# Performance work log

Measured on AMD Instinct MI355X. Metric: run time of the kernel, lower is better.

## Reference

```python
import jax, jax.numpy as jnp
import numpy as np


def setup_inputs() -> dict:
    key = jax.random.key(0)
    k1, k2, k3, k4 = jax.random.split(key, 4)
    N, E, F_IN, H, C = 100000, 1600000, 128, 64, 64
    x = jax.random.normal(k1, (N, F_IN), dtype=jnp.float32)
    edge_index = jax.random.randint(k2, (2, E), 0, N, dtype=jnp.int64)
    W1 = jax.random.normal(k3, (F_IN, H), dtype=jnp.float32) / np.sqrt(F_IN)
    b1 = jnp.zeros((H,), dtype=jnp.float32)
    W2 = jax.random.normal(k4, (H, C), dtype=jnp.float32) / np.sqrt(H)
    b2 = jnp.zeros((C,), dtype=jnp.float32)
    return {"x": x, "edge_index": edge_index, "W1": W1, "b1": b1, "W2": W2, "b2": b2}


def reference(x, edge_index, W1, b1, W2, b2):
    N = x.shape[0]
    # add self-loops (PyG GCNConv default)
    loop = jnp.arange(N, dtype=edge_index.dtype)
    src = jnp.concatenate([edge_index[0], loop])
    dst = jnp.concatenate([edge_index[1], loop])
    # symmetric normalization: deg^{-1/2}[src] * deg^{-1/2}[dst], deg over dst
    deg = jax.ops.segment_sum(jnp.ones_like(dst, dtype=x.dtype), dst, num_segments=N)
    dis = jnp.where(deg > 0, jax.lax.rsqrt(deg), 0.0)
    norm = dis[src] * dis[dst]  # [E+N]

    def gcn_conv(h, W, b):
        h = h @ W                                   # [N, out]
        msg = h[src] * norm[:, None]                # [E+N, out] gather
        agg = jax.ops.segment_sum(msg, dst, num_segments=N)  # scatter-add
        return agg + b

    h = jax.nn.relu(gcn_conv(x, W1, b1))
    # dropout inactive in eval mode
    out = gcn_conv(h, W2, b2)
    return jax.nn.log_softmax(out, axis=1)
```

## Files before the change

kernel.cpp:

```cpp
#include <hip/hip_runtime.h>
#include <cstdint>
#include <cstddef>

#define PASSA_EDGES 8192
#define PASSB_CAP   12288

typedef __attribute__((ext_vector_type(8))) short bf16x8;
typedef __attribute__((ext_vector_type(4))) float f32x4;


__device__ __forceinline__ unsigned short f2bf(float f) {
    unsigned int u = __float_as_uint(f);
    u += 0x7FFFu + ((u >> 16) & 1u);
    return (unsigned short)(u >> 16);
}
__device__ __forceinline__ float bf2f(unsigned short h) {
    return __uint_as_float((unsigned int)h << 16);
}

__device__ __forceinline__ void bf8_fma(uint4 u, float w, float* acc) {
    acc[0] += __uint_as_float(u.x << 16) * w;
    acc[1] += __uint_as_float(u.x & 0xFFFF0000u) * w;
    acc[2] += __uint_as_float(u.y << 16) * w;
    acc[3] += __uint_as_float(u.y & 0xFFFF0000u) * w;
    acc[4] += __uint_as_float(u.z << 16) * w;
    acc[5] += __uint_as_float(u.z & 0xFFFF0000u) * w;
    acc[6] += __uint_as_float(u.w << 16) * w;
    acc[7] += __uint_as_float(u.w & 0xFFFF0000u) * w;
}
__device__ __forceinline__ void bf8_unpack(uint4 u, float* v) {
    v[0] = __uint_as_float(u.x << 16);
    v[1] = __uint_as_float(u.x & 0xFFFF0000u);
    v[2] = __uint_as_float(u.y << 16);
    v[3] = __uint_as_float(u.y & 0xFFFF0000u);
    v[4] = __uint_as_float(u.z << 16);
    v[5] = __uint_as_float(u.z & 0xFFFF0000u);
    v[6] = __uint_as_float(u.w << 16);
    v[7] = __uint_as_float(u.w & 0xFFFF0000u);
}


__global__ void bcur_init(int* __restrict__ bcur, int NBUCK, int CAP) {
    int b = threadIdx.x;
    if (b < NBUCK) bcur[b] = b * CAP;
}


__global__ __launch_bounds__(256) void passA(const int* __restrict__ src,
                                             const int* __restrict__ dst,
                                             int* __restrict__ bcur,
                                             int2* __restrict__ bbuf, int E,
                                             int CAP, int shift) {
    __shared__ int2 bins[PASSA_EDGES];
    __shared__ int  cnt[256], off[256], cur[256], gbase[256];
    const int t  = threadIdx.x;
    const int e0 = blockIdx.x * PASSA_EDGES;
    const int n  = min(PASSA_EDGES, E - e0);

    cnt[t] = 0;
    __syncthreads();
    for (int i = t; i < n; i += 256) atomicAdd(&cnt[dst[e0 + i] >> shift], 1);
    __syncthreads();

    int v = cnt[t];
    off[t] = v;
    __syncthreads();
    for (int o = 1; o < 256; o <<= 1) {
        int u = (t >= o) ? off[t - o] : 0;
        __syncthreads();
        off[t] += u;
        __syncthreads();
    }
    int excl = off[t] - v;
    off[t]   = excl;
    cur[t]   = excl;
    __syncthreads();

    for (int i = t; i < n; i += 256) {
        int d = dst[e0 + i];
        int s = src[e0 + i];
        int p = atomicAdd(&cur[d >> shift], 1);
        bins[p] = make_int2(s, d);
    }
    if (cnt[t] > 0) gbase[t] = atomicAdd(&bcur[t], cnt[t]);
    __syncthreads();

    const int w = t >> 6, lane = t & 63;
    for (int b = w; b < 256; b += 4) {
        int c = cnt[b];
        if (c == 0) continue;
        int lo  = off[b], go = gbase[b];
        int lim = (b + 1) * CAP;
        if (go + c > lim) c = max(0, lim - go);
        for (int i = lane; i < c; i += 64) bbuf[go + i] = bins[lo + i];
    }
}


__global__ __launch_bounds__(256) void hist_dis(const int2* __restrict__ bbuf,
                                                const int* __restrict__ bcur,
                                                int* __restrict__ hist,
                                                float* __restrict__ dis,
                                                int N, int CAP, int shift) {
    __shared__ int cnt[1024];
    const int b     = blockIdx.x;
    const int node0 = b << shift;
    const int nn    = min(1 << shift, N - node0);
    for (int j = threadIdx.x; j < nn; j += 256) cnt[j] = 0;
    __syncthreads();
    const int start = b * CAP, end = bcur[b];
    for (int e = start + threadIdx.x; e < end; e += 256)
        atomicAdd(&cnt[bbuf[e].y - node0], 1);
    __syncthreads();
    for (int j = threadIdx.x; j < nn; j += 256) {
        int c = cnt[j];
        hist[node0 + j] = (c + 7) & ~7;
        dis[node0 + j]  = rsqrtf((float)(c + 1));
    }
}


__global__ __launch_bounds__(256) void scan_partial(const int* __restrict__ hist,
                                                    int* __restrict__ partials, int N) {
    __shared__ int red[256];
    const int t    = threadIdx.x;
    const int base = blockIdx.x * 1024 + t * 4;
    int s = 0;
    if (base + 3 < N) {
        int4 v = *(const int4*)&hist[base];
        s = v.x + v.y + v.z + v.w;
    } else {
        for (int i = 0; i < 4; i++)
            if (base + i < N) s += hist[base + i];
    }
    red[t] = s;
    __syncthreads();
    for (int off = 128; off; off >>= 1) {
        if (t < off) red[t] += red[t + off];
        __syncthreads();
    }
    if (t == 0) partials[blockIdx.x] = red[0];
}

__global__ __launch_bounds__(256) void scan_offsets(int* __restrict__ partials, int NB) {
    __shared__ int tmp[256];
    const int t = threadIdx.x;
    int v = (t < NB) ? partials[t] : 0;
    tmp[t] = v;
    __syncthreads();
    for (int off = 1; off < 256; off <<= 1) {
        int u = (t >= off) ? tmp[t - off] : 0;
        __syncthreads();
        tmp[t] += u;
        __syncthreads();
    }
    if (t < NB) partials[t] = tmp[t] - v;
}

__global__ __launch_bounds__(256) void scan_apply(const int* __restrict__ hist,
                                                  const int* __restrict__ partials,
                                                  int* __restrict__ ptr, int N) {
    __shared__ int tsum[256];
    const int t    = threadIdx.x;
    const int base = blockIdx.x * 1024 + t * 4;
    int v[4];
    int s = 0;
    for (int i = 0; i < 4; i++) {
        v[i] = (base + i < N) ? hist[base + i] : 0;
        s += v[i];
    }
    tsum[t] = s;
    __syncthreads();
    for (int off = 1; off < 256; off <<= 1) {
        int u = (t >= off) ? tsum[t - off] : 0;
        __syncthreads();
        tsum[t] += u;
        __syncthreads();
    }
    int run = partials[blockIdx.x] + tsum[t] - s;
    for (int i = 0; i < 4; i++) {
        if (base + i < N) {
            ptr[base + i] = run;
            run += v[i];
        }
    }
    if (base <= N - 1 && N - 1 < base + 4) ptr[N] = run;
}


__global__ __launch_bounds__(256) void passB(const int2* __restrict__ bbuf,
                                             const int* __restrict__ bcur,
                                             const int* __restrict__ ptr,
                                             int2* __restrict__ csrw,
                                             const float* __restrict__ dis,
                                             int N, int CAP, int shift) {
    __shared__ int lcnt[1024];
    __shared__ int lcsr[PASSB_CAP];
    const int b     = blockIdx.x;
    const int node0 = b << shift;
    const int nn    = min(1 << shift, N - node0);
    const int cbase = ptr[node0];
    const int csize = ptr[node0 + nn] - cbase;

    for (int j = threadIdx.x; j < nn; j += 256) lcnt[j] = ptr[node0 + j] - cbase;
    __syncthreads();

    const int start = b * CAP, end = bcur[b];
    if (csize <= PASSB_CAP) {
        for (int i = threadIdx.x; i < csize; i += 256) lcsr[i] = -1;
        __syncthreads();
        for (int e = start + threadIdx.x; e < end; e += 256) {
            int2 pr = bbuf[e];
            int  p  = atomicAdd(&lcnt[pr.y - node0], 1);
            lcsr[p] = pr.x;
        }
        __syncthreads();
        for (int i = threadIdx.x; i < csize; i += 256) {
            int s = lcsr[i];
            csrw[cbase + i] = (s < 0) ? make_int2(0, 0)
                                      : make_int2(s, __float_as_int(dis[s]));
        }
    } else {
        for (int i = threadIdx.x; i < csize; i += 256) csrw[cbase + i] = make_int2(0, 0);
        __syncthreads();
        for (int e = start + threadIdx.x; e < end; e += 256) {
            int2 pr = bbuf[e];
            int  p  = atomicAdd(&lcnt[pr.y - node0], 1);
            csrw[cbase + p] = make_int2(pr.x, __float_as_int(dis[pr.x]));
        }
    }
}


__global__ __launch_bounds__(256) void prep_wfrag(const float* __restrict__ W1,
                                                  const float* __restrict__ W2,
                                                  unsigned short* __restrict__ whi1,
                                                  unsigned short* __restrict__ wlo1,
                                                  unsigned short* __restrict__ whi2,
                                                  unsigned short* __restrict__ wlo2) {
    for (int e = threadIdx.x; e < 128 * 64; e += 256) {
        const int blk = e >> 9, l = (e >> 3) & 63, j = e & 7;
        const int k = (blk >> 2) * 32 + (l >> 4) * 8 + j;
        const int n = (blk & 3) * 16 + (l & 15);
        const float v = W1[k * 64 + n];
        const unsigned short h = f2bf(v);
        whi1[e] = h;
        wlo1[e] = f2bf(v - bf2f(h));
    }
    for (int e = threadIdx.x; e < 64 * 64; e += 256) {
        const int blk = e >> 9, l = (e >> 3) & 63, j = e & 7;
        const int k = (blk >> 2) * 32 + (l >> 4) * 8 + j;
        const int n = (blk & 3) * 16 + (l & 15);
        const float v = W2[k * 64 + n];
        const unsigned short h = f2bf(v);
        whi2[e] = h;
        wlo2[e] = f2bf(v - bf2f(h));
    }
}


template <int K>
__global__ __launch_bounds__(256) void gemm_mfma(const float* __restrict__ X,
                                                 const unsigned short* __restrict__ whi,
                                                 const unsigned short* __restrict__ wlo,
                                                 unsigned short* __restrict__ Yb, int N) {
    constexpr int LDX = K + 4;
    __shared__ float xs[64 * LDX];
    const int tid  = threadIdx.x;
    const int row0 = blockIdx.x * 64;

#pragma unroll
    for (int i = 0; i < (64 * K) / 1024; ++i) {
        const int fidx = i * 1024 + tid * 4;
        const int r = fidx / K, c = fidx % K;
        const float4 v = *(const float4*)(X + (size_t)min(row0 + r, N - 1) * K + c);
        *(float4*)&xs[r * LDX + c] = v;
    }
    __syncthreads();

    const int w = tid >> 6, l = tid & 63;
    const int m = l & 15, kg = l >> 4;

    f32x4 acc[4] = {};
    const float* xrow = &xs[(w * 16 + m) * LDX];

#pragma unroll
    for (int s = 0; s < K / 32; ++s) {
        const float4 a0 = *(const float4*)(xrow + s * 32 + kg * 8);
        const float4 a1 = *(const float4*)(xrow + s * 32 + kg * 8 + 4);
        const float av[8] = {a0.x, a0.y, a0.z, a0.w, a1.x, a1.y, a1.z, a1.w};
        bf16x8 ahi, alo;
#pragma unroll
        for (int j = 0; j < 8; ++j) {
            const unsigned short h = f2bf(av[j]);
            ahi[j] = (short)h;
            alo[j] = (short)f2bf(av[j] - bf2f(h));
        }
#pragma unroll
        for (int nt = 0; nt < 4; ++nt) {
            const bf16x8 bh = *(const bf16x8*)&whi[(s * 4 + nt) * 512 + l * 8];
            const bf16x8 bl = *(const bf16x8*)&wlo[(s * 4 + nt) * 512 + l * 8];
            acc[nt] = __builtin_amdgcn_mfma_f32_16x16x32_bf16(ahi, bh, acc[nt], 0, 0, 0);
            acc[nt] = __builtin_amdgcn_mfma_f32_16x16x32_bf16(alo, bh, acc[nt], 0, 0, 0);
            acc[nt] = __builtin_amdgcn_mfma_f32_16x16x32_bf16(ahi, bl, acc[nt], 0, 0, 0);
        }
    }

#pragma unroll
    for (int nt = 0; nt < 4; ++nt)
#pragma unroll
        for (int r = 0; r < 4; ++r) {
            const int row = row0 + w * 16 + kg * 4 + r;
            if (row < N) Yb[(size_t)row * 64 + nt * 16 + m] = f2bf(acc[nt][r]);
        }
}


__device__ __forceinline__ void gather8_pad(const unsigned short* __restrict__ B,
                                            const int2* __restrict__ csrw,
                                            int s0, int iters, int co, float* acc) {
    const int4* cs = (const int4*)(csrw + s0);
    int4 c0 = make_int4(0, 0, 0, 0), c1 = c0, c2 = c0, c3 = c0;
    if (iters > 0) { c0 = cs[0]; c1 = cs[1]; c2 = cs[2]; c3 = cs[3]; }
    for (int it = 0; it < iters; ++it) {
        const int nb = min(it + 1, iters - 1) * 4;
        int4 n0 = cs[nb], n1 = cs[nb + 1], n2 = cs[nb + 2], n3 = cs[nb + 3];
        uint4 u0 = *(const uint4*)&B[(size_t)c0.x * 64 + co * 8];
        uint4 u1 = *(const uint4*)&B[(size_t)c0.z * 64 + co * 8];
        uint4 u2 = *(const uint4*)&B[(size_t)c1.x * 64 + co * 8];
        uint4 u3 = *(const uint4*)&B[(size_t)c1.z * 64 + co * 8];
        uint4 u4 = *(const uint4*)&B[(size_t)c2.x * 64 + co * 8];
        uint4 u5 = *(const uint4*)&B[(size_t)c2.z * 64 + co * 8];
        uint4 u6 = *(const uint4*)&B[(size_t)c3.x * 64 + co * 8];
        uint4 u7 = *(const uint4*)&B[(size_t)c3.z * 64 + co * 8];
        bf8_fma(u0, __int_as_float(c0.y), acc);
        bf8_fma(u1, __int_as_float(c0.w), acc);
        bf8_fma(u2, __int_as_float(c1.y), acc);
        bf8_fma(u3, __int_as_float(c1.w), acc);
        bf8_fma(u4, __int_as_float(c2.y), acc);
        bf8_fma(u5, __int_as_float(c2.w), acc);
        bf8_fma(u6, __int_as_float(c3.y), acc);
        bf8_fma(u7, __int_as_float(c3.w), acc);
        c0 = n0; c1 = n1; c2 = n2; c3 = n3;
    }
}


__global__ __launch_bounds__(256) void agg_l1(const unsigned short* __restrict__ B,
                                              const int2* __restrict__ csrw,
                                              const int* __restrict__ ptr,
                                              const float* __restrict__ dis,
                                              const float* __restrict__ b1,
                                              float* __restrict__ hs, int N) {
    const int wid  = threadIdx.x >> 6;
    const int lane = threadIdx.x & 63;
    const int eg   = lane >> 3;
    const int co   = lane & 7;

    const int  row = blockIdx.x * 32 + wid * 8 + eg;
    const bool hr  = (row < N);

    const int   s0 = hr ? ptr[row] : 0;
    const int   s1 = hr ? ptr[row + 1] : 0;
    const float di = hr ? dis[row] : 0.f;
    const int   iters = (s1 - s0) >> 3;

    float acc[8] = {};
    gather8_pad(B, csrw, s0, iters, co, acc);

    if (!hr) return;

    uint4 us = *(const uint4*)&B[(size_t)row * 64 + co * 8];
    float bs[8];
    bf8_unpack(us, bs);
    float bb[8];
    *(float4*)&bb[0] = *(const float4*)&b1[co * 8];
    *(float4*)&bb[4] = *(const float4*)&b1[co * 8 + 4];

    float h[8];
#pragma unroll
    for (int i = 0; i < 8; i++)
        h[i] = fmaxf((acc[i] + bs[i] * di) * di + bb[i], 0.f);

    *(float4*)&hs[(size_t)row * 64 + co * 8]     = make_float4(h[0], h[1], h[2], h[3]);
    *(float4*)&hs[(size_t)row * 64 + co * 8 + 4] = make_float4(h[4], h[5], h[6], h[7]);
}


__global__ __launch_bounds__(256) void agg_l2(const unsigned short* __restrict__ B,
                                              const int2* __restrict__ csrw,
                                              const int* __restrict__ ptr,
                                              const float* __restrict__ dis,
                                              const float* __restrict__ b2,
                                              float* __restrict__ out, int N) {
    const int wid  = threadIdx.x >> 6;
    const int lane = threadIdx.x & 63;
    const int eg   = lane >> 3;
    const int co   = lane & 7;

    const int  row = blockIdx.x * 32 + wid * 8 + eg;
    const bool hr  = (row < N);

    const int   s0 = hr ? ptr[row] : 0;
    const int   s1 = hr ? ptr[row + 1] : 0;
    const float di = hr ? dis[row] : 0.f;
    const int   iters = (s1 - s0) >> 3;

    float acc[8] = {};
    gather8_pad(B, csrw, s0, iters, co, acc);

    if (!hr) return;

    uint4 us = *(const uint4*)&B[(size_t)row * 64 + co * 8];
    float bs[8];
    bf8_unpack(us, bs);
    float bb[8];
    *(float4*)&bb[0] = *(const float4*)&b2[co * 8];
    *(float4*)&bb[4] = *(const float4*)&b2[co * 8 + 4];

    float v[8];
#pragma unroll
    for (int i = 0; i < 8; i++) v[i] = (acc[i] + bs[i] * di) * di + bb[i];

    float m = v[0];
#pragma unroll
    for (int i = 1; i < 8; i++) m = fmaxf(m, v[i]);
#pragma unroll
    for (int off = 1; off <= 4; off <<= 1) m = fmaxf(m, __shfl_xor(m, off));
    float s = 0.f;
#pragma unroll
    for (int i = 0; i < 8; i++) s += __expf(v[i] - m);
#pragma unroll
    for (int off = 1; off <= 4; off <<= 1) s += __shfl_xor(s, off);
    float lse = m + __logf(s);

    float4 oa = make_float4(v[0] - lse, v[1] - lse, v[2] - lse, v[3] - lse);
    float4 ob = make_float4(v[4] - lse, v[5] - lse, v[6] - lse, v[7] - lse);
    *(float4*)&out[(size_t)row * 64 + co * 8]     = oa;
    *(float4*)&out[(size_t)row * 64 + co * 8 + 4] = ob;
}


extern "C" void kernel_launch(void* const* d_in, const int* in_sizes, int n_in,
                              void* d_out, int out_size, void* d_ws, size_t ws_size,
                              hipStream_t stream) {
    const float* x   = (const float*)d_in[0];
    const int*   ei  = (const int*)d_in[1];
    const float* W1  = (const float*)d_in[2];
    const float* b1  = (const float*)d_in[3];
    const float* W2  = (const float*)d_in[4];
    const float* b2  = (const float*)d_in[5];
    float*       out = (float*)d_out;

    const int  N   = in_sizes[0] / 128;
    const int  E   = in_sizes[1] / 2;
    const int* src = ei;
    const int* dst = ei + E;
    const int  NB  = (N + 1023) / 1024;

    int shift = 9;
    while (((N - 1) >> shift) >= 256) shift++;
    const int NBUCK = ((N - 1) >> shift) + 1;
    const int CAP   = ((E / NBUCK) * 3 / 2 + 255) & ~255;

    auto align256 = [](size_t v) { return (v + 255) & ~(size_t)255; };
    char*           p        = (char*)d_ws;
    float*          dis      = (float*)p;          p += align256((size_t)N * 4);
    int*            ptr      = (int*)p;            p += align256((size_t)(N + 1) * 4);
    int*            hist     = (int*)p;            p += align256((size_t)N * 4);
    int*            partials = (int*)p;            p += align256((size_t)NB * 4);
    int*            bcur     = (int*)p;            p += align256(256 * 4);
    int2*           csrw     = (int2*)p;           p += align256(((size_t)E + 8 * (size_t)N) * 8);
    int2*           bbuf     = (int2*)p;           p += align256((size_t)NBUCK * CAP * 8);
    unsigned short* xwb      = (unsigned short*)p; p += align256((size_t)N * 64 * 2);
    unsigned short* whi1     = (unsigned short*)p; p += align256(128 * 64 * 2);
    unsigned short* wlo1     = (unsigned short*)p; p += align256(128 * 64 * 2);
    unsigned short* whi2     = (unsigned short*)p; p += align256(64 * 64 * 2);
    unsigned short* wlo2     = (unsigned short*)p; p += align256(64 * 64 * 2);

    float* hs = out;

    bcur_init<<<1, 256, 0, stream>>>(bcur, NBUCK, CAP);
    prep_wfrag<<<1, 256, 0, stream>>>(W1, W2, whi1, wlo1, whi2, wlo2);
    passA<<<(E + PASSA_EDGES - 1) / PASSA_EDGES, 256, 0, stream>>>(src, dst, bcur, bbuf, E, CAP, shift);
    hist_dis<<<NBUCK, 256, 0, stream>>>(bbuf, bcur, hist, dis, N, CAP, shift);
    scan_partial<<<NB, 256, 0, stream>>>(hist, partials, N);
    scan_offsets<<<1, 256, 0, stream>>>(partials, NB);
    scan_apply<<<NB, 256, 0, stream>>>(hist, partials, ptr, N);
    passB<<<NBUCK, 256, 0, stream>>>(bbuf, bcur, ptr, csrw, dis, N, CAP, shift);

    gemm_mfma<128><<<(N + 63) / 64, 256, 0, stream>>>(x, whi1, wlo1, xwb, N);
    agg_l1<<<(N + 31) / 32, 256, 0, stream>>>(xwb, csrw, ptr, dis, b1, hs, N);
    gemm_mfma<64><<<(N + 63) / 64, 256, 0, stream>>>(hs, whi2, wlo2, xwb, N);
    agg_l2<<<(N + 31) / 32, 256, 0, stream>>>(xwb, csrw, ptr, dis, b2, out, N);
}
```

Measured before the change: 266.9 us.

## Replace bucketed two-pass CSR build with global-atomic histogram and direct scatter

Drops the two-level bucket sort (passA into buckets, then passB into CSR in shared memory) and instead builds the degree histogram with global atomics on dst, scans it, and scatters each edge straight into its CSR slot with a global atomic cursor. Padding slots are zeroed by a separate per-node kernel, and the dis computation is folded into the scan. This removes the intermediate bucket buffer and its write/read traffic, in exchange for many random global atomics and scattered 8-byte writes. It also makes neighbor order within a row nondeterministic.

```diff
diff --git a/kernel.cpp b/kernel.cpp
--- a/kernel.cpp
+++ b/kernel.cpp
@@ -1,9 +1,6 @@
 #include <hip/hip_runtime.h>
 #include <cstdint>
 #include <cstddef>
-
-#define PASSA_EDGES 8192
-#define PASSB_CAP   12288
 
 typedef __attribute__((ext_vector_type(8))) short bf16x8;
 typedef __attribute__((ext_vector_type(4))) float f32x4;
@@ -40,98 +37,40 @@
 }
 
 
-__global__ void bcur_init(int* __restrict__ bcur, int NBUCK, int CAP) {
-    int b = threadIdx.x;
-    if (b < NBUCK) bcur[b] = b * CAP;
-}
-
-
-__global__ __launch_bounds__(256) void passA(const int* __restrict__ src,
-                                             const int* __restrict__ dst,
-                                             int* __restrict__ bcur,
-                                             int2* __restrict__ bbuf, int E,
-                                             int CAP, int shift) {
-    __shared__ int2 bins[PASSA_EDGES];
-    __shared__ int  cnt[256], off[256], cur[256], gbase[256];
-    const int t  = threadIdx.x;
-    const int e0 = blockIdx.x * PASSA_EDGES;
-    const int n  = min(PASSA_EDGES, E - e0);
-
-    cnt[t] = 0;
-    __syncthreads();
-    for (int i = t; i < n; i += 256) atomicAdd(&cnt[dst[e0 + i] >> shift], 1);
-    __syncthreads();
-
-    int v = cnt[t];
-    off[t] = v;
-    __syncthreads();
-    for (int o = 1; o < 256; o <<= 1) {
-        int u = (t >= o) ? off[t - o] : 0;
-        __syncthreads();
-        off[t] += u;
-        __syncthreads();
-    }
-    int excl = off[t] - v;
-    off[t]   = excl;
-    cur[t]   = excl;
-    __syncthreads();
-
-    for (int i = t; i < n; i += 256) {
-        int d = dst[e0 + i];
-        int s = src[e0 + i];
-        int p = atomicAdd(&cur[d >> shift], 1);
-        bins[p] = make_int2(s, d);
-    }
-    if (cnt[t] > 0) gbase[t] = atomicAdd(&bcur[t], cnt[t]);
-    __syncthreads();
-
-    const int w = t >> 6, lane = t & 63;
-    for (int b = w; b < 256; b += 4) {
-        int c = cnt[b];
-        if (c == 0) continue;
-        int lo  = off[b], go = gbase[b];
-        int lim = (b + 1) * CAP;
-        if (go + c > lim) c = max(0, lim - go);
-        for (int i = lane; i < c; i += 64) bbuf[go + i] = bins[lo + i];
-    }
-}
-
-
-__global__ __launch_bounds__(256) void hist_dis(const int2* __restrict__ bbuf,
-                                                const int* __restrict__ bcur,
-                                                int* __restrict__ hist,
-                                                float* __restrict__ dis,
-                                                int N, int CAP, int shift) {
-    __shared__ int cnt[1024];
-    const int b     = blockIdx.x;
-    const int node0 = b << shift;
-    const int nn    = min(1 << shift, N - node0);
-    for (int j = threadIdx.x; j < nn; j += 256) cnt[j] = 0;
-    __syncthreads();
-    const int start = b * CAP, end = bcur[b];
-    for (int e = start + threadIdx.x; e < end; e += 256)
-        atomicAdd(&cnt[bbuf[e].y - node0], 1);
-    __syncthreads();
-    for (int j = threadIdx.x; j < nn; j += 256) {
-        int c = cnt[j];
-        hist[node0 + j] = (c + 7) & ~7;
-        dis[node0 + j]  = rsqrtf((float)(c + 1));
-    }
+__global__ __launch_bounds__(256) void zero_hist(int* __restrict__ hist, int N4) {
+    const int i = blockIdx.x * 256 + threadIdx.x;
+    if (i < N4) ((int4*)hist)[i] = make_int4(0, 0, 0, 0);
+}
+
+__global__ __launch_bounds__(256) void hist_build(const int* __restrict__ dst,
+                                                  int* __restrict__ hist, int E) {
+    const int stride = gridDim.x * 256;
+    for (int e = blockIdx.x * 256 + threadIdx.x; e < E; e += stride)
+        atomicAdd(&hist[dst[e]], 1);
 }
 
 
 __global__ __launch_bounds__(256) void scan_partial(const int* __restrict__ hist,
-                                                    int* __restrict__ partials, int N) {
+                                                    int* __restrict__ partials,
+                                                    float* __restrict__ dis, int N) {
     __shared__ int red[256];
     const int t    = threadIdx.x;
     const int base = blockIdx.x * 1024 + t * 4;
     int s = 0;
     if (base + 3 < N) {
         int4 v = *(const int4*)&hist[base];
-        s = v.x + v.y + v.z + v.w;
+        s = ((v.x + 7) & ~7) + ((v.y + 7) & ~7) + ((v.z + 7) & ~7) + ((v.w + 7) & ~7);
+        dis[base]     = rsqrtf((float)(v.x + 1));
+        dis[base + 1] = rsqrtf((float)(v.y + 1));
+        dis[base + 2] = rsqrtf((float)(v.z + 1));
+        dis[base + 3] = rsqrtf((float)(v.w + 1));
     } else {
         for (int i = 0; i < 4; i++)
-            if (base + i < N) s += hist[base + i];
+            if (base + i < N) {
+                int c = hist[base + i];
+                s += (c + 7) & ~7;
+                dis[base + i] = rsqrtf((float)(c + 1));
+            }
     }
     red[t] = s;
     __syncthreads();
@@ -157,16 +96,19 @@
     if (t < NB) partials[t] = tmp[t] - v;
 }
 
+
 __global__ __launch_bounds__(256) void scan_apply(const int* __restrict__ hist,
                                                   const int* __restrict__ partials,
-                                                  int* __restrict__ ptr, int N) {
+                                                  int* __restrict__ ptr,
+                                                  int* __restrict__ cur, int N) {
     __shared__ int tsum[256];
     const int t    = threadIdx.x;
     const int base = blockIdx.x * 1024 + t * 4;
     int v[4];
     int s = 0;
     for (int i = 0; i < 4; i++) {
-        v[i] = (base + i < N) ? hist[base + i] : 0;
+        int c = (base + i < N) ? hist[base + i] : 0;
+        v[i]  = (c + 7) & ~7;
         s += v[i];
     }
     tsum[t] = s;
@@ -181,6 +123,7 @@
     for (int i = 0; i < 4; i++) {
         if (base + i < N) {
             ptr[base + i] = run;
+            cur[base + i] = run;
             run += v[i];
         }
     }
@@ -188,46 +131,28 @@
 }
 
 
-__global__ __launch_bounds__(256) void passB(const int2* __restrict__ bbuf,
-                                             const int* __restrict__ bcur,
-                                             const int* __restrict__ ptr,
-                                             int2* __restrict__ csrw,
-                                             const float* __restrict__ dis,
-                                             int N, int CAP, int shift) {
-    __shared__ int lcnt[1024];
-    __shared__ int lcsr[PASSB_CAP];
-    const int b     = blockIdx.x;
-    const int node0 = b << shift;
-    const int nn    = min(1 << shift, N - node0);
-    const int cbase = ptr[node0];
-    const int csize = ptr[node0 + nn] - cbase;
-
-    for (int j = threadIdx.x; j < nn; j += 256) lcnt[j] = ptr[node0 + j] - cbase;
-    __syncthreads();
-
-    const int start = b * CAP, end = bcur[b];
-    if (csize <= PASSB_CAP) {
-        for (int i = threadIdx.x; i < csize; i += 256) lcsr[i] = -1;
-        __syncthreads();
-        for (int e = start + threadIdx.x; e < end; e += 256) {
-            int2 pr = bbuf[e];
-            int  p  = atomicAdd(&lcnt[pr.y - node0], 1);
-            lcsr[p] = pr.x;
-        }
-        __syncthreads();
-        for (int i = threadIdx.x; i < csize; i += 256) {
-            int s = lcsr[i];
-            csrw[cbase + i] = (s < 0) ? make_int2(0, 0)
-                                      : make_int2(s, __float_as_int(dis[s]));
-        }
-    } else {
-        for (int i = threadIdx.x; i < csize; i += 256) csrw[cbase + i] = make_int2(0, 0);
-        __syncthreads();
-        for (int e = start + threadIdx.x; e < end; e += 256) {
-            int2 pr = bbuf[e];
-            int  p  = atomicAdd(&lcnt[pr.y - node0], 1);
-            csrw[cbase + p] = make_int2(pr.x, __float_as_int(dis[pr.x]));
-        }
+__global__ __launch_bounds__(256) void pad_fill(const int* __restrict__ hist,
+                                                const int* __restrict__ ptr,
+                                                int2* __restrict__ csrw, int N) {
+    const int j = blockIdx.x * 256 + threadIdx.x;
+    if (j >= N) return;
+    const int t0 = ptr[j] + hist[j];
+    const int t1 = ptr[j + 1];
+    for (int p = t0; p < t1; ++p) csrw[p] = make_int2(0, 0);
+}
+
+
+__global__ __launch_bounds__(256) void scatter_csr(const int* __restrict__ src,
+                                                   const int* __restrict__ dst,
+                                                   const float* __restrict__ dis,
+                                                   int* __restrict__ cur,
+                                                   int2* __restrict__ csrw, int E) {
+    const int stride = gridDim.x * 256;
+    for (int e = blockIdx.x * 256 + threadIdx.x; e < E; e += stride) {
+        const int d = dst[e];
+        const int s = src[e];
+        const int p = atomicAdd(&cur[d], 1);
+        csrw[p] = make_int2(s, __float_as_int(dis[s]));
     }
 }
 
@@ -457,21 +382,17 @@
     const int* src = ei;
     const int* dst = ei + E;
     const int  NB  = (N + 1023) / 1024;
-
-    int shift = 9;
-    while (((N - 1) >> shift) >= 256) shift++;
-    const int NBUCK = ((N - 1) >> shift) + 1;
-    const int CAP   = ((E / NBUCK) * 3 / 2 + 255) & ~255;
+    const int  N4  = (N + 3) / 4;
+    const int  EB  = min((E + 255) / 256, 2048);
 
     auto align256 = [](size_t v) { return (v + 255) & ~(size_t)255; };
     char*           p        = (char*)d_ws;
     float*          dis      = (float*)p;          p += align256((size_t)N * 4);
     int*            ptr      = (int*)p;            p += align256((size_t)(N + 1) * 4);
     int*            hist     = (int*)p;            p += align256((size_t)N * 4);
+    int*            cur      = (int*)p;            p += align256((size_t)N * 4);
     int*            partials = (int*)p;            p += align256((size_t)NB * 4);
-    int*            bcur     = (int*)p;            p += align256(256 * 4);
     int2*           csrw     = (int2*)p;           p += align256(((size_t)E + 8 * (size_t)N) * 8);
-    int2*           bbuf     = (int2*)p;           p += align256((size_t)NBUCK * CAP * 8);
     unsigned short* xwb      = (unsigned short*)p; p += align256((size_t)N * 64 * 2);
     unsigned short* whi1     = (unsigned short*)p; p += align256(128 * 64 * 2);
     unsigned short* wlo1     = (unsigned short*)p; p += align256(128 * 64 * 2);
@@ -480,14 +401,14 @@
 
     float* hs = out;
 
-    bcur_init<<<1, 256, 0, stream>>>(bcur, NBUCK, CAP);
+    zero_hist<<<(N4 + 255) / 256, 256, 0, stream>>>(hist, N4);
     prep_wfrag<<<1, 256, 0, stream>>>(W1, W2, whi1, wlo1, whi2, wlo2);
-    passA<<<(E + PASSA_EDGES - 1) / PASSA_EDGES, 256, 0, stream>>>(src, dst, bcur, bbuf, E, CAP, shift);
-    hist_dis<<<NBUCK, 256, 0, stream>>>(bbuf, bcur, hist, dis, N, CAP, shift);
-    scan_partial<<<NB, 256, 0, stream>>>(hist, partials, N);
+    hist_build<<<EB, 256, 0, stream>>>(dst, hist, E);
+    scan_partial<<<NB, 256, 0, stream>>>(hist, partials, dis, N);
     scan_offsets<<<1, 256, 0, stream>>>(partials, NB);
-    scan_apply<<<NB, 256, 0, stream>>>(hist, partials, ptr, N);
-    passB<<<NBUCK, 256, 0, stream>>>(bbuf, bcur, ptr, csrw, dis, N, CAP, shift);
+    scan_apply<<<NB, 256, 0, stream>>>(hist, partials, ptr, cur, N);
+    pad_fill<<<(N + 255) / 256, 256, 0, stream>>>(hist, ptr, csrw, N);
+    scatter_csr<<<EB, 256, 0, stream>>>(src, dst, dis, cur, csrw, E);
 
     gemm_mfma<128><<<(N + 63) / 64, 256, 0, stream>>>(x, whi1, wlo1, xwb, N);
     agg_l1<<<(N + 31) / 32, 256, 0, stream>>>(xwb, csrw, ptr, dis, b1, hs, N);
```

New measurement: 375.6 us. 40.7% more time.
